# Kernel optimization log

Hardware: AMD Instinct MI355X
Metric: run time of the kernel (lower is better)

Reference implementation:

```python
import jax, jax.numpy as jnp
import numpy as np

B, T, C, H = 8, 2048, 1024, 64

def setup_inputs() -> dict:
    key = jax.random.key(0)
    k1, k2, k3, k4 = jax.random.split(key, 4)
    return {
        "inputs": jax.random.normal(k1, (B, T, C), dtype=jnp.float32),
        "Wq": jax.random.normal(k2, (C, H), dtype=jnp.float32) * (C ** -0.5),
        "Wk": jax.random.normal(k3, (C, H), dtype=jnp.float32) * (C ** -0.5),
        "Wv": jax.random.normal(k4, (C, H), dtype=jnp.float32) * (C ** -0.5),
    }

def reference(inputs, Wq, Wk, Wv):
    # q,k,v: [B,T,H]
    q = jnp.einsum('btc,ch->bth', inputs, Wq)
    k = jnp.einsum('btc,ch->bth', inputs, Wk)
    v = jnp.einsum('btc,ch->bth', inputs, Wv)
    c = inputs.shape[-1]
    # NOTE: original scales by C**-0.5 (embedding dim), not head_size**-0.5
    scale = jnp.asarray(c, inputs.dtype) ** -0.5
    wei = jnp.einsum('bqh,bkh->bqk', q, k) * scale  # [B,T,T]
    t = inputs.shape[1]
    causal = jnp.tril(jnp.ones((t, t), dtype=bool))
    wei = jnp.where(causal[None, :, :], wei, -jnp.inf)
    wei = jax.nn.softmax(wei, axis=-1)
    # dropout is identity in eval / DROP_RATE=0
    out = jnp.einsum('bqk,bkh->bqh', wei, v)  # [B,T,H]
    return out
```

## Files before the change

kernel.cpp:

```cpp
#include <hip/hip_runtime.h>
#include <stdint.h>

#define B_ 8
#define T_ 2048
#define C_ 1024
#define H_ 64
#define M_ (B_*T_)

typedef __bf16 bf16x8 __attribute__((ext_vector_type(8)));
typedef float  f32x4  __attribute__((ext_vector_type(4)));

union U4B { uint4 u; bf16x8 v; };

__device__ __forceinline__ unsigned short f32_to_bf16(float f) {
    union { float f; uint32_t u; } c; c.f = f;
    uint32_t u = c.u;
    u += 0x7fffu + ((u >> 16) & 1u);
    return (unsigned short)(u >> 16);
}
__device__ __forceinline__ uint32_t pack2_bf16(float a, float b) {
#if __has_builtin(__builtin_amdgcn_cvt_pk_bf16_f32)
    typedef __bf16 bf16x2 __attribute__((ext_vector_type(2)));
    union { bf16x2 v; uint32_t u; } c;
    c.v = __builtin_amdgcn_cvt_pk_bf16_f32(a, b);
    return c.u;
#else
    return (uint32_t)f32_to_bf16(a) | ((uint32_t)f32_to_bf16(b) << 16);
#endif
}

__global__ __launch_bounds__(256) void prepack_w(const float* __restrict__ Wq,
        const float* __restrict__ Wk, const float* __restrict__ Wv,
        unsigned short* __restrict__ wpk) {
    int o = blockIdx.x * 256 + threadIdx.x;
    if (o >= 24576) return;
    int lane = o & 63, nt = (o >> 6) % 12, kc = o / (64 * 12);
    int l15 = lane & 15, grp = lane >> 4;
    int n = nt * 16 + l15;
    int k = kc * 32 + grp * 8;
    const float* W = (n < 64) ? Wq : (n < 128) ? Wk : Wv;
    int col = n & 63;
    unsigned short tmp[8];
    #pragma unroll
    for (int j = 0; j < 8; j++) tmp[j] = f32_to_bf16(W[(size_t)(k + j) * 64 + col]);
    *(uint4*)(wpk + (size_t)o * 8) = *(uint4*)tmp;
}

__global__ __launch_bounds__(256) void qkv_kernel(const float* __restrict__ X,
        const unsigned short* __restrict__ wpk,
        unsigned short* __restrict__ qb, unsigned short* __restrict__ kb,
        unsigned short* __restrict__ vt) {
    __shared__ unsigned short Xl[16 * 1024];
    const int tid = threadIdx.x;
    const int wave = tid >> 6, lane = tid & 63;
    const int grp = lane >> 4, l15 = lane & 15;
    const int h = wave;
    const int t16 = blockIdx.x;

    const unsigned short* wp = wpk + ((size_t)(h * 3) * 64 + lane) * 8;
    uint4 w[4][3];
    #pragma unroll
    for (int d = 0; d < 4; d++)
        #pragma unroll
        for (int jj = 0; jj < 3; jj++)
            w[d][jj] = *(const uint4*)(wp + ((size_t)d * 768 + jj * 64) * 8);

    {
        const int rr = tid >> 4, ch = tid & 15;
        const float* xrow = X + ((size_t)t16 * 16 + rr) * 1024 + ch * 8;
        float4 xa[8], xb[8];
        #pragma unroll
        for (int i = 0; i < 8; i++) {
            xa[i] = *(const float4*)(xrow + i * 128);
            xb[i] = *(const float4*)(xrow + i * 128 + 4);
        }
        char* xd = (char*)Xl + rr * 2048;
        #pragma unroll
        for (int i = 0; i < 8; i++) {
            uint4 pk = (uint4){ pack2_bf16(xa[i].x, xa[i].y), pack2_bf16(xa[i].z, xa[i].w),
                                pack2_bf16(xb[i].x, xb[i].y), pack2_bf16(xb[i].z, xb[i].w) };
            int colb = (ch * 16 + i * 256) ^ ((rr & 7) << 4);
            *(uint4*)(xd + colb) = pk;
        }
    }
    __syncthreads();

    f32x4 acc[3];
    #pragma unroll
    for (int j = 0; j < 3; j++) acc[j] = (f32x4){0.f, 0.f, 0.f, 0.f};

    const char* xs = (const char*)Xl + l15 * 2048;
    const int xswz = (l15 & 7) << 4;

    U4B xr0, xr1, xr2;
    xr0.u = *(const uint4*)(xs + ((0 * 64 + grp * 16) ^ xswz));
    xr1.u = *(const uint4*)(xs + ((1 * 64 + grp * 16) ^ xswz));
    xr2.u = *(const uint4*)(xs + ((2 * 64 + grp * 16) ^ xswz));

    #pragma unroll
    for (int kc = 0; kc < 32; kc++) {
        const int q = kc & 3;
        U4B a = (kc % 3 == 0) ? xr0 : (kc % 3 == 1) ? xr1 : xr2;
        U4B b0, b1, b2;
        b0.u = w[q][0]; b1.u = w[q][1]; b2.u = w[q][2];
        acc[0] = __builtin_amdgcn_mfma_f32_16x16x32_bf16(a.v, b0.v, acc[0], 0, 0, 0);
        acc[1] = __builtin_amdgcn_mfma_f32_16x16x32_bf16(a.v, b1.v, acc[1], 0, 0, 0);
        acc[2] = __builtin_amdgcn_mfma_f32_16x16x32_bf16(a.v, b2.v, acc[2], 0, 0, 0);
        if (kc + 3 < 32) {
            U4B t;
            t.u = *(const uint4*)(xs + (((kc + 3) * 64 + grp * 16) ^ xswz));
            if (kc % 3 == 0) xr0 = t; else if (kc % 3 == 1) xr1 = t; else xr2 = t;
        }
        if (kc + 4 < 32) {
            const unsigned short* wn = wp + ((size_t)(kc + 4) * 768) * 8;
            #pragma unroll
            for (int jj = 0; jj < 3; jj++)
                w[q][jj] = *(const uint4*)(wn + jj * 64 * 8);
        }
    }

    const int r0 = t16 * 16 + grp * 4;
    const int bb = r0 >> 11;
    const int t0 = r0 & 2047;
    #pragma unroll
    for (int jj = 0; jj < 3; jj++) {
        int col = (h * 3 + jj) * 16 + l15;
        if (col < 64) {
            for (int r = 0; r < 4; r++)
                qb[(size_t)(r0 + r) * 64 + col] = f32_to_bf16(acc[jj][r] * 0.03125f);
        } else if (col < 128) {
            for (int r = 0; r < 4; r++)
                kb[(size_t)(r0 + r) * 64 + (col - 64)] = f32_to_bf16(acc[jj][r]);
        } else {
            int c = col - 128;
            ushort4 vv;
            vv.x = f32_to_bf16(acc[jj][0]); vv.y = f32_to_bf16(acc[jj][1]);
            vv.z = f32_to_bf16(acc[jj][2]); vv.w = f32_to_bf16(acc[jj][3]);
            *(ushort4*)(vt + ((size_t)bb * 64 + c) * 2048 + t0) = vv;
        }
    }
}

__global__ __launch_bounds__(256) void attn1_kernel(const unsigned short* __restrict__ qb,
        const unsigned short* __restrict__ kb, const unsigned short* __restrict__ vt,
        float* __restrict__ pl, float* __restrict__ pacc) {
    __shared__ unsigned short Kl[64][72];
    __shared__ unsigned short Vl[64][72];
    const int tid = threadIdx.x;
    const int wave = tid >> 6, lane = tid & 63;
    const int grp = lane >> 4, l15 = lane & 15;
    const int b = blockIdx.x & 7;
    int f = blockIdx.x >> 3;
    int g = 0;
    for (; g < 32; g++) { int c = (35 - g) >> 2; if (f < c) break; f -= c; }
    const int j = 31 - g;
    const int s = f;
    const int ktend = min(4, (j + 1) - 4 * s);
    const int qbase = j * 64 + wave * 16;

    const unsigned short* qp = qb + ((size_t)b * 2048 + qbase + l15) * 64 + grp * 8;
    bf16x8 bq0 = *(const bf16x8*)qp;
    bf16x8 bq1 = *(const bf16x8*)(qp + 32);

    float lsum = 0.f;
    f32x4 acc[4];
    for (int d = 0; d < 4; d++) acc[d] = (f32x4){0.f, 0.f, 0.f, 0.f};

    const unsigned short* kB = kb + ((size_t)b * 2048 + s * 256) * 64;
    const unsigned short* vB = vt + (size_t)b * 64 * 2048 + s * 256;
    const int r1 = tid >> 3, c1 = (tid & 7) * 8;
    const int r2 = (tid + 256) >> 3, c2 = c1;

    uint4 kr0, kr1, vr0, vr1;
    kr0 = *(const uint4*)(kB + (size_t)r1 * 64 + c1);
    kr1 = *(const uint4*)(kB + (size_t)r2 * 64 + c2);
    vr0 = *(const uint4*)(vB + (size_t)r1 * 2048 + c1);
    vr1 = *(const uint4*)(vB + (size_t)r2 * 2048 + c2);

    for (int kt = 0; kt < ktend; kt++) {
        *(uint4*)&Kl[r1][c1] = kr0;  *(uint4*)&Kl[r2][c2] = kr1;
        *(uint4*)&Vl[r1][c1] = vr0;  *(uint4*)&Vl[r2][c2] = vr1;
        __syncthreads();
        if (kt + 1 < ktend) {
            const unsigned short* kN = kB + (size_t)(kt + 1) * 64 * 64;
            const unsigned short* vN = vB + (kt + 1) * 64;
            kr0 = *(const uint4*)(kN + (size_t)r1 * 64 + c1);
            kr1 = *(const uint4*)(kN + (size_t)r2 * 64 + c2);
            vr0 = *(const uint4*)(vN + (size_t)r1 * 2048 + c1);
            vr1 = *(const uint4*)(vN + (size_t)r2 * 2048 + c2);
        }
        const int keybase = s * 256 + kt * 64;
        f32x4 st[4];
        #pragma unroll
        for (int nt = 0; nt < 4; nt++) {
            bf16x8 a0 = *(const bf16x8*)&Kl[nt * 16 + l15][grp * 8];
            bf16x8 a1 = *(const bf16x8*)&Kl[nt * 16 + l15][32 + grp * 8];
            f32x4 t = (f32x4){0.f, 0.f, 0.f, 0.f};
            t = __builtin_amdgcn_mfma_f32_16x16x32_bf16(a0, bq0, t, 0, 0, 0);
            t = __builtin_amdgcn_mfma_f32_16x16x32_bf16(a1, bq1, t, 0, 0, 0);
            st[nt] = t;
        }
        if (keybase + 63 > qbase) {
            int q = qbase + l15;
            #pragma unroll
            for (int nt = 0; nt < 4; nt++)
                for (int r = 0; r < 4; r++)
                    if (keybase + nt * 16 + grp * 4 + r > q) st[nt][r] = -1e30f;
        }
        float p[4][4];
        #pragma unroll
        for (int nt = 0; nt < 4; nt++)
            for (int r = 0; r < 4; r++) { p[nt][r] = __expf(st[nt][r]); lsum += p[nt][r]; }
        uint32_t t0a = pack2_bf16(p[0][0], p[0][1]), t0b = pack2_bf16(p[0][2], p[0][3]);
        uint32_t t1a = pack2_bf16(p[1][0], p[1][1]), t1b = pack2_bf16(p[1][2], p[1][3]);
        uint32_t t2a = pack2_bf16(p[2][0], p[2][1]), t2b = pack2_bf16(p[2][2], p[2][3]);
        uint32_t t3a = pack2_bf16(p[3][0], p[3][1]), t3b = pack2_bf16(p[3][2], p[3][3]);
        const int s0l = ((grp & 1) << 5) + l15, s1l = s0l + 16;
        const bool hi = (grp >= 2);
        U4B bw0, bw1;
        {
            uint32_t e0a = (uint32_t)__shfl((int)t0a, s0l, 64);
            uint32_t e0b = (uint32_t)__shfl((int)t0b, s0l, 64);
            uint32_t e0c = (uint32_t)__shfl((int)t0a, s1l, 64);
            uint32_t e0d = (uint32_t)__shfl((int)t0b, s1l, 64);
            uint32_t e1a = (uint32_t)__shfl((int)t1a, s0l, 64);
            uint32_t e1b = (uint32_t)__shfl((int)t1b, s0l, 64);
            uint32_t e1c = (uint32_t)__shfl((int)t1a, s1l, 64);
            uint32_t e1d = (uint32_t)__shfl((int)t1b, s1l, 64);
            bw0.u = (uint4){ hi ? e1a : e0a, hi ? e1b : e0b, hi ? e1c : e0c, hi ? e1d : e0d };
        }
        {
            uint32_t e0a = (uint32_t)__shfl((int)t2a, s0l, 64);
            uint32_t e0b = (uint32_t)__shfl((int)t2b, s0l, 64);
            uint32_t e0c = (uint32_t)__shfl((int)t2a, s1l, 64);
            uint32_t e0d = (uint32_t)__shfl((int)t2b, s1l, 64);
            uint32_t e1a = (uint32_t)__shfl((int)t3a, s0l, 64);
            uint32_t e1b = (uint32_t)__shfl((int)t3b, s0l, 64);
            uint32_t e1c = (uint32_t)__shfl((int)t3a, s1l, 64);
            uint32_t e1d = (uint32_t)__shfl((int)t3b, s1l, 64);
            bw1.u = (uint4){ hi ? e1a : e0a, hi ? e1b : e0b, hi ? e1c : e0c, hi ? e1d : e0d };
        }
        #pragma unroll
        for (int dt = 0; dt < 4; dt++) {
            bf16x8 av0 = *(const bf16x8*)&Vl[dt * 16 + l15][grp * 8];
            bf16x8 av1 = *(const bf16x8*)&Vl[dt * 16 + l15][32 + grp * 8];
            acc[dt] = __builtin_amdgcn_mfma_f32_16x16x32_bf16(av0, bw0.v, acc[dt], 0, 0, 0);
            acc[dt] = __builtin_amdgcn_mfma_f32_16x16x32_bf16(av1, bw1.v, acc[dt], 0, 0, 0);
        }
        __syncthreads();
    }
    lsum += __shfl_xor(lsum, 16, 64);
    lsum += __shfl_xor(lsum, 32, 64);
    size_t rowq = (size_t)b * 2048 + qbase + l15;
    size_t p = rowq * 8 + s;
    if (grp == 0) pl[p] = lsum;
    #pragma unroll
    for (int dt = 0; dt < 4; dt++)
        *(f32x4*)&pacc[p * 64 + dt * 16 + grp * 4] = acc[dt];
}

__global__ __launch_bounds__(256) void attn2_kernel(const float* __restrict__ pl,
        const float* __restrict__ pacc, float* __restrict__ out) {
    int idx = blockIdx.x * 256 + threadIdx.x;
    int row = idx >> 4;
    int d0 = (idx & 15) * 4;
    int t = row & 2047;
    int ns = ((t >> 6) + 4) >> 2;
    float den = 0.f;
    f32x4 num = (f32x4){0.f, 0.f, 0.f, 0.f};
    for (int s = 0; s < ns; s++) {
        den += pl[(size_t)row * 8 + s];
        num += *(const f32x4*)&pacc[((size_t)row * 8 + s) * 64 + d0];
    }
    float inv = 1.f / den;
    *(f32x4*)&out[(size_t)row * 64 + d0] = num * inv;
}

extern "C" void kernel_launch(void* const* d_in, const int* in_sizes, int n_in,
                              void* d_out, int out_size, void* d_ws, size_t ws_size,
                              hipStream_t stream) {
    const float* X  = (const float*)d_in[0];
    const float* Wq = (const float*)d_in[1];
    const float* Wk = (const float*)d_in[2];
    const float* Wv = (const float*)d_in[3];
    float* out = (float*)d_out;

    unsigned short* qb  = (unsigned short*)d_ws;
    unsigned short* kb  = qb + (size_t)M_ * 64;
    unsigned short* wpk = kb + (size_t)M_ * 64;
    unsigned short* vt  = wpk + (size_t)24576 * 8;
    float* pl   = (float*)(vt + (size_t)B_ * 64 * 2048);
    float* pacc = pl + (size_t)M_ * 8;

    prepack_w<<<96, 256, 0, stream>>>(Wq, Wk, Wv, wpk);
    qkv_kernel<<<1024, 256, 0, stream>>>(X, wpk, qb, kb, vt);
    attn1_kernel<<<1152, 256, 0, stream>>>(qb, kb, vt, pl, pacc);
    attn2_kernel<<<1024, 256, 0, stream>>>(pl, pacc, out);
}
```

Before: 133.2 us.

## Load X tile directly to LDS as fp32 and convert to bf16 at use

The QKV projection kernel now stages the fp32 input tile straight into shared memory with global_load_lds, bypassing registers, and keeps it in fp32 with an XOR swizzle. Each wave then reads fp32 pairs from LDS and packs them to bf16 just before every MFMA. This is meant to remove the register round trip and the up-front conversion pass in the load phase. In exchange it doubles LDS use to 64KB per block, which may limit occupancy, doubles LDS read traffic, and repeats conversion work inside the MFMA loop.

```diff
diff --git a/kernel.cpp b/kernel.cpp
--- a/kernel.cpp
+++ b/kernel.cpp
@@ -50,7 +50,7 @@
         const unsigned short* __restrict__ wpk,
         unsigned short* __restrict__ qb, unsigned short* __restrict__ kb,
         unsigned short* __restrict__ vt) {
-    __shared__ unsigned short Xl[16 * 1024];
+    __shared__ float Xl[16 * 1024];
     const int tid = threadIdx.x;
     const int wave = tid >> 6, lane = tid & 63;
     const int grp = lane >> 4, l15 = lane & 15;
@@ -63,24 +63,19 @@
     for (int d = 0; d < 4; d++)
         #pragma unroll
         for (int jj = 0; jj < 3; jj++)
-            w[d][jj] = *(const uint4*)(wp + ((size_t)d * 768 + jj * 64) * 8);
+            w[d][jj] = *(const uint4*)(wp + (size_t)(d * 768 + jj * 64) * 8);
 
     {
-        const int rr = tid >> 4, ch = tid & 15;
-        const float* xrow = X + ((size_t)t16 * 16 + rr) * 1024 + ch * 8;
-        float4 xa[8], xb[8];
-        #pragma unroll
-        for (int i = 0; i < 8; i++) {
-            xa[i] = *(const float4*)(xrow + i * 128);
-            xb[i] = *(const float4*)(xrow + i * 128 + 4);
-        }
-        char* xd = (char*)Xl + rr * 2048;
-        #pragma unroll
-        for (int i = 0; i < 8; i++) {
-            uint4 pk = (uint4){ pack2_bf16(xa[i].x, xa[i].y), pack2_bf16(xa[i].z, xa[i].w),
-                                pack2_bf16(xb[i].x, xb[i].y), pack2_bf16(xb[i].z, xb[i].w) };
-            int colb = (ch * 16 + i * 256) ^ ((rr & 7) << 4);
-            *(uint4*)(xd + colb) = pk;
+        const char* xbase = (const char*)(X + (size_t)t16 * 16 * 1024);
+        #pragma unroll
+        for (int i = 0; i < 16; i++) {
+            const int row = wave * 4 + (i >> 2);
+            const int colb = (((i & 3) * 1024) + lane * 16) ^ ((row & 7) << 4);
+            const char* src = xbase + (size_t)row * 4096 + colb;
+            char* dst = (char*)Xl + wave * 16384 + i * 1024;
+            __builtin_amdgcn_global_load_lds(
+                (const __attribute__((address_space(1))) uint32_t*)src,
+                (__attribute__((address_space(3))) uint32_t*)dst, 16, 0, 0);
         }
     }
     __syncthreads();
@@ -89,30 +84,38 @@
     #pragma unroll
     for (int j = 0; j < 3; j++) acc[j] = (f32x4){0.f, 0.f, 0.f, 0.f};
 
-    const char* xs = (const char*)Xl + l15 * 2048;
-    const int xswz = (l15 & 7) << 4;
-
-    U4B xr0, xr1, xr2;
-    xr0.u = *(const uint4*)(xs + ((0 * 64 + grp * 16) ^ xswz));
-    xr1.u = *(const uint4*)(xs + ((1 * 64 + grp * 16) ^ xswz));
-    xr2.u = *(const uint4*)(xs + ((2 * 64 + grp * 16) ^ xswz));
+    const char* xs = (const char*)Xl + l15 * 4096;
+    const int xsw = (l15 & 7) << 4;
+    const int o0 = (grp * 32) ^ xsw;
+    const int o1 = (grp * 32 + 16) ^ xsw;
+
+    float4 xA0, xB0, xA1, xB1, xA2, xB2;
+    xA0 = *(const float4*)(xs + 0 * 128 + o0);  xB0 = *(const float4*)(xs + 0 * 128 + o1);
+    xA1 = *(const float4*)(xs + 1 * 128 + o0);  xB1 = *(const float4*)(xs + 1 * 128 + o1);
+    xA2 = *(const float4*)(xs + 2 * 128 + o0);  xB2 = *(const float4*)(xs + 2 * 128 + o1);
 
     #pragma unroll
     for (int kc = 0; kc < 32; kc++) {
         const int q = kc & 3;
-        U4B a = (kc % 3 == 0) ? xr0 : (kc % 3 == 1) ? xr1 : xr2;
+        float4 fa = (kc % 3 == 0) ? xA0 : (kc % 3 == 1) ? xA1 : xA2;
+        float4 fb = (kc % 3 == 0) ? xB0 : (kc % 3 == 1) ? xB1 : xB2;
+        U4B a;
+        a.u = (uint4){ pack2_bf16(fa.x, fa.y), pack2_bf16(fa.z, fa.w),
+                       pack2_bf16(fb.x, fb.y), pack2_bf16(fb.z, fb.w) };
         U4B b0, b1, b2;
         b0.u = w[q][0]; b1.u = w[q][1]; b2.u = w[q][2];
         acc[0] = __builtin_amdgcn_mfma_f32_16x16x32_bf16(a.v, b0.v, acc[0], 0, 0, 0);
         acc[1] = __builtin_amdgcn_mfma_f32_16x16x32_bf16(a.v, b1.v, acc[1], 0, 0, 0);
         acc[2] = __builtin_amdgcn_mfma_f32_16x16x32_bf16(a.v, b2.v, acc[2], 0, 0, 0);
         if (kc + 3 < 32) {
-            U4B t;
-            t.u = *(const uint4*)(xs + (((kc + 3) * 64 + grp * 16) ^ xswz));
-            if (kc % 3 == 0) xr0 = t; else if (kc % 3 == 1) xr1 = t; else xr2 = t;
+            float4 ta = *(const float4*)(xs + (kc + 3) * 128 + o0);
+            float4 tb = *(const float4*)(xs + (kc + 3) * 128 + o1);
+            if (kc % 3 == 0)      { xA0 = ta; xB0 = tb; }
+            else if (kc % 3 == 1) { xA1 = ta; xB1 = tb; }
+            else                  { xA2 = ta; xB2 = tb; }
         }
         if (kc + 4 < 32) {
-            const unsigned short* wn = wp + ((size_t)(kc + 4) * 768) * 8;
+            const unsigned short* wn = wp + (size_t)(kc + 4) * 768 * 8;
             #pragma unroll
             for (int jj = 0; jj < 3; jj++)
                 w[q][jj] = *(const uint4*)(wn + jj * 64 * 8);
```

Result: no change. 135.7 us (+1.8%).
